# Performance work log

Measured on AMD Instinct MI355X. Metric: run time of the kernel, lower is better.

The kernel has to match this reference:

```python
import jax, jax.numpy as jnp
import numpy as np

# Module config (matches init_kwargs)
SHAPE = (32, 32)          # wire grid
KERNEL = (3, 3)           # window per dim
NUM_LAYERS = 4
NINPUTS = int(np.prod(KERNEL))        # 9
NPOS = 2 ** NINPUTS                   # 512 possible boolean input combos


def _bitmask():
    # itertools.product(range(2), repeat=NINPUTS) then transpose -> (NINPUTS, NPOS)
    # combination j, window-element m has bit (j >> (NINPUTS-1-m)) & 1
    j = jnp.arange(NPOS)
    m = jnp.arange(NINPUTS)
    return ((j[None, :] >> (NINPUTS - 1 - m)[:, None]) & 1).astype(jnp.float32)


def _convolve(x):
    # x: (B, H, W) -> (B, H, W, K) wrapped sliding windows (im2col via rolls),
    # faithful to ASIC.convolve with kernel_offset='center'.
    out = x
    for d, k in enumerate(KERNEL):
        # window element i along dim d comes from position +i (wraparound)
        out = jnp.stack([jnp.roll(out, -i, axis=1 + d) for i in range(k)], axis=out.ndim)
    out = out.reshape(x.shape + (-1,))  # (B, H, W, K) with k0 slowest-varying
    # 'center' offset: roll by prod((k-1)//2) along the LAST spatial dim (as the torch code does)
    shift = int(np.prod([(k - 1) // 2 for k in KERNEL]))
    out = jnp.roll(out, shift, axis=len(KERNEL))  # axis = last spatial axis in (B, H, W, K)
    return out


def setup_inputs() -> dict:
    key = jax.random.key(0)
    k1, k2 = jax.random.split(key)
    x = jax.random.uniform(k1, (16,) + SHAPE, dtype=jnp.float32)
    toggle_gates = jax.random.uniform(k2, (NUM_LAYERS, NPOS) + SHAPE, dtype=jnp.float32)
    return {"x": x, "toggle_gates": toggle_gates}


def reference(x, toggle_gates):
    tw = jax.nn.sigmoid(toggle_gates)       # (L, NPOS, H, W)
    bits = _bitmask()                        # (NINPUTS, NPOS)
    # embed(): shape == x spatial shape -> stride-1 slices; initial state is x, output is full state
    state = x                                # (B, H, W)
    for layer in range(NUM_LAYERS):
        conv = _convolve(state)              # (B, H, W, K)
        # soft-LUT weights: prod over window elems of (1 - |bit - input|)
        w = jnp.prod(1.0 - jnp.abs(conv[..., None] - bits), axis=-2)  # (B, H, W, NPOS)
        state = jnp.clip(jnp.einsum('bhwp,phw->bhw', w, tw[layer]), 0.0, 1.0)
    return state
```

## Files before the change

### kernel.cpp

```cpp
#include <hip/hip_runtime.h>

#define HH 32
#define WW 32
#define NPOS 512
#define TILE 8
#define PPAD 516
#define NTHR 256
#define RPAD 33

__device__ __forceinline__ void make_v(const float c[9], float* v) {
    float a2[2], a4[4], a8[8], a16[16];
    a2[0] = 1.0f - c[4]; a2[1] = c[4];
    #pragma unroll
    for (int i = 0; i < 2; ++i)  { a4[2*i]  = a2[i]  * (1.0f - c[5]); a4[2*i+1]  = a2[i]  * c[5]; }
    #pragma unroll
    for (int i = 0; i < 4; ++i)  { a8[2*i]  = a4[i]  * (1.0f - c[6]); a8[2*i+1]  = a4[i]  * c[6]; }
    #pragma unroll
    for (int i = 0; i < 8; ++i)  { a16[2*i] = a8[i]  * (1.0f - c[7]); a16[2*i+1] = a8[i]  * c[7]; }
    #pragma unroll
    for (int i = 0; i < 16; ++i) { v[2*i]   = a16[i] * (1.0f - c[8]); v[2*i+1]   = a16[i] * c[8]; }
}

__global__ __launch_bounds__(NTHR) void asic_layer(
    const float* __restrict__ src,
    const float* __restrict__ tg,
    float* __restrict__ dst)
{
    __shared__ float  lut[TILE * PPAD];
    __shared__ float2 red[8 * RPAD];

    const int t     = threadIdx.x;
    const int sp    = blockIdx.x & 127;
    const int bhalf = blockIdx.x >> 7;
    const int hw0   = sp * TILE;

    #pragma unroll
    for (int k = 0; k < 16; ++k) {
        int f   = t + NTHR * k;
        int p   = f >> 3;
        int pos = f & 7;
        float g = tg[p * (HH * WW) + hw0 + pos];
        lut[pos * PPAD + p] = 1.0f / (1.0f + __expf(-g));
    }

    const int hwl = t & 7;
    const int bp  = (t >> 3) & 3;
    const int oct = t >> 5;
    const int h   = hw0 >> 5;
    const int w   = (hw0 & 31) + hwl;
    const int b0  = bhalf * 8 + 2 * bp;

    float c0[9], c1[9];
    const float* s0 = src + b0 * (HH * WW);
    const float* s1 = s0 + (HH * WW);
    #pragma unroll
    for (int i = 0; i < 3; ++i) {
        int row = ((h + i) & 31) * 32;
        #pragma unroll
        for (int j = 0; j < 3; ++j) {
            int idx = row + ((w + j - 1 + 32) & 31);
            c0[3 * i + j] = s0[idx];
            c1[3 * i + j] = s1[idx];
        }
    }

    __syncthreads();

    float v0[32], v1[32];
    make_v(c0, v0);
    make_v(c1, v1);

    const int bit0 = (oct >> 2) & 1, bit1 = (oct >> 1) & 1, bit2 = oct & 1;
    float base0 = (bit0 ? c0[0] : 1.0f - c0[0]) * (bit1 ? c0[1] : 1.0f - c0[1]) * (bit2 ? c0[2] : 1.0f - c0[2]);
    float base1 = (bit0 ? c1[0] : 1.0f - c1[0]) * (bit1 ? c1[1] : 1.0f - c1[1]) * (bit2 ? c1[2] : 1.0f - c1[2]);
    float uA0 = base0 * (1.0f - c0[3]), uB0 = base0 * c0[3];
    float uA1 = base1 * (1.0f - c1[3]), uB1 = base1 * c1[3];

    const float4* lutp = (const float4*)(lut + hwl * PPAD);
    const float4* A = lutp + (2 * oct) * 8;
    const float4* B = A + 8;

    float sA0 = 0.f, sA1 = 0.f, sB0 = 0.f, sB1 = 0.f;
    #pragma unroll
    for (int l4 = 0; l4 < 8; ++l4) {
        float4 LA = A[l4];
        float4 LB = B[l4];
        sA0 = fmaf(LA.x, v0[4*l4+0], sA0); sA0 = fmaf(LA.y, v0[4*l4+1], sA0);
        sA0 = fmaf(LA.z, v0[4*l4+2], sA0); sA0 = fmaf(LA.w, v0[4*l4+3], sA0);
        sA1 = fmaf(LA.x, v1[4*l4+0], sA1); sA1 = fmaf(LA.y, v1[4*l4+1], sA1);
        sA1 = fmaf(LA.z, v1[4*l4+2], sA1); sA1 = fmaf(LA.w, v1[4*l4+3], sA1);
        sB0 = fmaf(LB.x, v0[4*l4+0], sB0); sB0 = fmaf(LB.y, v0[4*l4+1], sB0);
        sB0 = fmaf(LB.z, v0[4*l4+2], sB0); sB0 = fmaf(LB.w, v0[4*l4+3], sB0);
        sB1 = fmaf(LB.x, v1[4*l4+0], sB1); sB1 = fmaf(LB.y, v1[4*l4+1], sB1);
        sB1 = fmaf(LB.z, v1[4*l4+2], sB1); sB1 = fmaf(LB.w, v1[4*l4+3], sB1);
    }
    float acc0 = fmaf(uA0, sA0, uB0 * sB0);
    float acc1 = fmaf(uA1, sA1, uB1 * sB1);

    red[oct * RPAD + bp * 8 + hwl] = make_float2(acc0, acc1);
    __syncthreads();

    if (t < 64) {
        int hw  = t & 7;
        int bl  = t >> 3;
        int bpi = bl >> 1, par = bl & 1;
        float s = 0.0f;
        #pragma unroll
        for (int o = 0; o < 8; ++o) {
            float2 r = red[o * RPAD + bpi * 8 + hw];
            s += par ? r.y : r.x;
        }
        s = fminf(fmaxf(s, 0.0f), 1.0f);
        int b = bhalf * 8 + bl;
        dst[b * (HH * WW) + h * 32 + (hw0 & 31) + hw] = s;
    }
}

extern "C" void kernel_launch(void* const* d_in, const int* in_sizes, int n_in,
                              void* d_out, int out_size, void* d_ws, size_t ws_size,
                              hipStream_t stream) {
    const float* x  = (const float*)d_in[0];
    const float* tg = (const float*)d_in[1];
    float* out = (float*)d_out;
    float* ws  = (float*)d_ws;

    const int grid = 256;
    const size_t L = (size_t)NPOS * HH * WW;

    asic_layer<<<grid, NTHR, 0, stream>>>(x,   tg + 0 * L, ws);
    asic_layer<<<grid, NTHR, 0, stream>>>(ws,  tg + 1 * L, out);
    asic_layer<<<grid, NTHR, 0, stream>>>(out, tg + 2 * L, ws);
    asic_layer<<<grid, NTHR, 0, stream>>>(ws,  tg + 3 * L, out);
}
```

Measured before the change: 76.30 us.

## Fuse four layer launches into one persistent kernel with grid barriers

Replaces four per-layer launches with a single persistent kernel of 128 blocks by 512 threads. Each block preloads the sigmoid LUTs for all four layers into shared memory up front and synchronises layers through an atomic-counter grid barrier, with cross-block state passed through device-scope loads and stores. The aim is to remove three launch gaps and overlap all LUT loading, at the cost of a memset, barrier spin latency, a large shared-memory footprint and half as many blocks. The barrier is only safe if all 128 blocks are co-resident.

```diff
diff --git a/kernel.cpp b/kernel.cpp
--- a/kernel.cpp
+++ b/kernel.cpp
@@ -5,8 +5,28 @@
 #define NPOS 512
 #define TILE 8
 #define PPAD 516
-#define NTHR 256
+#define NTHR 512
+#define NBLK 128
+#define NLAYERS 4
 #define RPAD 33
+
+__device__ __forceinline__ float ld_dev(const float* p) {
+    return __hip_atomic_load(p, __ATOMIC_RELAXED, __HIP_MEMORY_SCOPE_AGENT);
+}
+__device__ __forceinline__ void st_dev(float* p, float v) {
+    __hip_atomic_store(p, v, __ATOMIC_RELAXED, __HIP_MEMORY_SCOPE_AGENT);
+}
+
+__device__ __forceinline__ void grid_barrier(int* cnt) {
+    __syncthreads();
+    if (threadIdx.x == 0) {
+        __hip_atomic_fetch_add(cnt, 1, __ATOMIC_RELAXED, __HIP_MEMORY_SCOPE_AGENT);
+        while (__hip_atomic_load(cnt, __ATOMIC_RELAXED, __HIP_MEMORY_SCOPE_AGENT) < NBLK) {
+            __builtin_amdgcn_s_sleep(8);
+        }
+    }
+    __syncthreads();
+}
 
 __device__ __forceinline__ void make_v(const float c[9], float* v) {
     float a2[2], a4[4], a8[8], a16[16];
@@ -21,98 +41,113 @@
     for (int i = 0; i < 16; ++i) { v[2*i]   = a16[i] * (1.0f - c[8]); v[2*i+1]   = a16[i] * c[8]; }
 }
 
-__global__ __launch_bounds__(NTHR) void asic_layer(
-    const float* __restrict__ src,
+__global__ __launch_bounds__(NTHR) void asic_fused(
+    const float* __restrict__ x,
     const float* __restrict__ tg,
-    float* __restrict__ dst)
+    float* __restrict__ bufA,
+    float* __restrict__ bufB,
+    float* __restrict__ out,
+    int* __restrict__ bar)
 {
-    __shared__ float  lut[TILE * PPAD];
-    __shared__ float2 red[8 * RPAD];
+    __shared__ float  lut[NLAYERS][TILE * PPAD];
+    __shared__ float2 red[2][8 * RPAD];
 
     const int t     = threadIdx.x;
-    const int sp    = blockIdx.x & 127;
-    const int bhalf = blockIdx.x >> 7;
-    const int hw0   = sp * TILE;
+    const int hw0   = blockIdx.x * TILE;
+    const int h     = hw0 >> 5;
+    const int w0    = hw0 & 31;
 
     #pragma unroll
-    for (int k = 0; k < 16; ++k) {
-        int f   = t + NTHR * k;
-        int p   = f >> 3;
-        int pos = f & 7;
-        float g = tg[p * (HH * WW) + hw0 + pos];
-        lut[pos * PPAD + p] = 1.0f / (1.0f + __expf(-g));
+    for (int k = 0; k < 32; ++k) {
+        int f     = t + NTHR * k;
+        int layer = f >> 12;
+        int r     = f & 4095;
+        int p     = r >> 3;
+        int pos   = r & 7;
+        float g = tg[(size_t)layer * NPOS * HH * WW + p * (HH * WW) + hw0 + pos];
+        lut[layer][pos * PPAD + p] = __builtin_amdgcn_rcpf(1.0f + __expf(-g));
     }
 
-    const int hwl = t & 7;
-    const int bp  = (t >> 3) & 3;
-    const int oct = t >> 5;
-    const int h   = hw0 >> 5;
-    const int w   = (hw0 & 31) + hwl;
-    const int b0  = bhalf * 8 + 2 * bp;
-
-    float c0[9], c1[9];
-    const float* s0 = src + b0 * (HH * WW);
-    const float* s1 = s0 + (HH * WW);
-    #pragma unroll
-    for (int i = 0; i < 3; ++i) {
-        int row = ((h + i) & 31) * 32;
-        #pragma unroll
-        for (int j = 0; j < 3; ++j) {
-            int idx = row + ((w + j - 1 + 32) & 31);
-            c0[3 * i + j] = s0[idx];
-            c1[3 * i + j] = s1[idx];
-        }
-    }
-
-    __syncthreads();
-
-    float v0[32], v1[32];
-    make_v(c0, v0);
-    make_v(c1, v1);
+    const int th    = t & 255;
+    const int bhalf = t >> 8;
+    const int hwl   = th & 7;
+    const int bp    = (th >> 3) & 3;
+    const int oct   = th >> 5;
+    const int w     = w0 + hwl;
+    const int b0    = bhalf * 8 + 2 * bp;
 
     const int bit0 = (oct >> 2) & 1, bit1 = (oct >> 1) & 1, bit2 = oct & 1;
-    float base0 = (bit0 ? c0[0] : 1.0f - c0[0]) * (bit1 ? c0[1] : 1.0f - c0[1]) * (bit2 ? c0[2] : 1.0f - c0[2]);
-    float base1 = (bit0 ? c1[0] : 1.0f - c1[0]) * (bit1 ? c1[1] : 1.0f - c1[1]) * (bit2 ? c1[2] : 1.0f - c1[2]);
-    float uA0 = base0 * (1.0f - c0[3]), uB0 = base0 * c0[3];
-    float uA1 = base1 * (1.0f - c1[3]), uB1 = base1 * c1[3];
 
-    const float4* lutp = (const float4*)(lut + hwl * PPAD);
-    const float4* A = lutp + (2 * oct) * 8;
-    const float4* B = A + 8;
+    const float* src = x;
 
-    float sA0 = 0.f, sA1 = 0.f, sB0 = 0.f, sB1 = 0.f;
-    #pragma unroll
-    for (int l4 = 0; l4 < 8; ++l4) {
-        float4 LA = A[l4];
-        float4 LB = B[l4];
-        sA0 = fmaf(LA.x, v0[4*l4+0], sA0); sA0 = fmaf(LA.y, v0[4*l4+1], sA0);
-        sA0 = fmaf(LA.z, v0[4*l4+2], sA0); sA0 = fmaf(LA.w, v0[4*l4+3], sA0);
-        sA1 = fmaf(LA.x, v1[4*l4+0], sA1); sA1 = fmaf(LA.y, v1[4*l4+1], sA1);
-        sA1 = fmaf(LA.z, v1[4*l4+2], sA1); sA1 = fmaf(LA.w, v1[4*l4+3], sA1);
-        sB0 = fmaf(LB.x, v0[4*l4+0], sB0); sB0 = fmaf(LB.y, v0[4*l4+1], sB0);
-        sB0 = fmaf(LB.z, v0[4*l4+2], sB0); sB0 = fmaf(LB.w, v0[4*l4+3], sB0);
-        sB1 = fmaf(LB.x, v1[4*l4+0], sB1); sB1 = fmaf(LB.y, v1[4*l4+1], sB1);
-        sB1 = fmaf(LB.z, v1[4*l4+2], sB1); sB1 = fmaf(LB.w, v1[4*l4+3], sB1);
-    }
-    float acc0 = fmaf(uA0, sA0, uB0 * sB0);
-    float acc1 = fmaf(uA1, sA1, uB1 * sB1);
+    for (int layer = 0; layer < NLAYERS; ++layer) {
+        float* dst = (layer == 3) ? out : ((layer & 1) ? bufB : bufA);
 
-    red[oct * RPAD + bp * 8 + hwl] = make_float2(acc0, acc1);
-    __syncthreads();
+        float c0[9], c1[9];
+        const float* s0 = src + b0 * (HH * WW);
+        const float* s1 = s0 + (HH * WW);
+        #pragma unroll
+        for (int i = 0; i < 3; ++i) {
+            int row = ((h + i) & 31) * 32;
+            #pragma unroll
+            for (int j = 0; j < 3; ++j) {
+                int idx = row + ((w + j - 1 + 32) & 31);
+                c0[3 * i + j] = ld_dev(s0 + idx);
+                c1[3 * i + j] = ld_dev(s1 + idx);
+            }
+        }
 
-    if (t < 64) {
-        int hw  = t & 7;
-        int bl  = t >> 3;
-        int bpi = bl >> 1, par = bl & 1;
-        float s = 0.0f;
+        if (layer == 0) __syncthreads();
+
+        float v0[32], v1[32];
+        make_v(c0, v0);
+        make_v(c1, v1);
+
+        float base0 = (bit0 ? c0[0] : 1.0f - c0[0]) * (bit1 ? c0[1] : 1.0f - c0[1]) * (bit2 ? c0[2] : 1.0f - c0[2]);
+        float base1 = (bit0 ? c1[0] : 1.0f - c1[0]) * (bit1 ? c1[1] : 1.0f - c1[1]) * (bit2 ? c1[2] : 1.0f - c1[2]);
+        float uA0 = base0 * (1.0f - c0[3]), uB0 = base0 * c0[3];
+        float uA1 = base1 * (1.0f - c1[3]), uB1 = base1 * c1[3];
+
+        const float4* lutp = (const float4*)(&lut[layer][0] + hwl * PPAD);
+        const float4* A = lutp + (2 * oct) * 8;
+        const float4* B = A + 8;
+        float sA0 = 0.f, sA1 = 0.f, sB0 = 0.f, sB1 = 0.f;
         #pragma unroll
-        for (int o = 0; o < 8; ++o) {
-            float2 r = red[o * RPAD + bpi * 8 + hw];
-            s += par ? r.y : r.x;
+        for (int l4 = 0; l4 < 8; ++l4) {
+            float4 LA = A[l4];
+            float4 LB = B[l4];
+            sA0 = fmaf(LA.x, v0[4*l4+0], sA0); sA0 = fmaf(LA.y, v0[4*l4+1], sA0);
+            sA0 = fmaf(LA.z, v0[4*l4+2], sA0); sA0 = fmaf(LA.w, v0[4*l4+3], sA0);
+            sA1 = fmaf(LA.x, v1[4*l4+0], sA1); sA1 = fmaf(LA.y, v1[4*l4+1], sA1);
+            sA1 = fmaf(LA.z, v1[4*l4+2], sA1); sA1 = fmaf(LA.w, v1[4*l4+3], sA1);
+            sB0 = fmaf(LB.x, v0[4*l4+0], sB0); sB0 = fmaf(LB.y, v0[4*l4+1], sB0);
+            sB0 = fmaf(LB.z, v0[4*l4+2], sB0); sB0 = fmaf(LB.w, v0[4*l4+3], sB0);
+            sB1 = fmaf(LB.x, v1[4*l4+0], sB1); sB1 = fmaf(LB.y, v1[4*l4+1], sB1);
+            sB1 = fmaf(LB.z, v1[4*l4+2], sB1); sB1 = fmaf(LB.w, v1[4*l4+3], sB1);
         }
-        s = fminf(fmaxf(s, 0.0f), 1.0f);
-        int b = bhalf * 8 + bl;
-        dst[b * (HH * WW) + h * 32 + (hw0 & 31) + hw] = s;
+        float acc0 = fmaf(uA0, sA0, uB0 * sB0);
+        float acc1 = fmaf(uA1, sA1, uB1 * sB1);
+
+        if (layer > 0) __syncthreads();
+        red[bhalf][oct * RPAD + bp * 8 + hwl] = make_float2(acc0, acc1);
+        __syncthreads();
+
+        if (th < 64) {
+            int hw  = th & 7;
+            int bl  = th >> 3;
+            int bpi = bl >> 1, par = bl & 1;
+            float s = 0.0f;
+            #pragma unroll
+            for (int o = 0; o < 8; ++o) {
+                float2 r = red[bhalf][o * RPAD + bpi * 8 + hw];
+                s += par ? r.y : r.x;
+            }
+            s = fminf(fmaxf(s, 0.0f), 1.0f);
+            st_dev(dst + (size_t)(bhalf * 8 + bl) * (HH * WW) + h * 32 + w0 + hw, s);
+        }
+
+        if (layer < NLAYERS - 1) grid_barrier(bar + layer);
+        src = dst;
     }
 }
 
@@ -121,14 +156,11 @@
                               hipStream_t stream) {
     const float* x  = (const float*)d_in[0];
     const float* tg = (const float*)d_in[1];
-    float* out = (float*)d_out;
-    float* ws  = (float*)d_ws;
+    float* out  = (float*)d_out;
+    float* bufA = (float*)d_ws;
+    float* bufB = bufA + 16 * HH * WW;
+    int*   bar  = (int*)((char*)d_ws + 256 * 1024);
 
-    const int grid = 256;
-    const size_t L = (size_t)NPOS * HH * WW;
-
-    asic_layer<<<grid, NTHR, 0, stream>>>(x,   tg + 0 * L, ws);
-    asic_layer<<<grid, NTHR, 0, stream>>>(ws,  tg + 1 * L, out);
-    asic_layer<<<grid, NTHR, 0, stream>>>(out, tg + 2 * L, ws);
-    asic_layer<<<grid, NTHR, 0, stream>>>(ws,  tg + 3 * L, out);
+    hipMemsetAsync(bar, 0, 4 * sizeof(int), stream);
+    asic_fused<<<NBLK, NTHR, 0, stream>>>(x, tg, bufA, bufB, out, bar);
 }
```

New measurement: 81.36 us. +6.6%, slower.
